# Kernel optimization log

Measured on AMD Instinct MI355X. Metric: run time of the kernel, lower is better.

Reference implementation:

```python
import jax, jax.numpy as jnp
import numpy as np

SEQ_LEN, HORIZON = 12, 12
B, N, DIN, DOUT, U = 16, 512, 2, 1, 64
NEG = -1e9


def _gat(x, W, a, b, mask):
    # x: (B, N, F_in); W: (F_in, G); a: (2, G); mask: (N, N) bool
    h = jnp.einsum('bnf,fg->bng', x, W)            # (B, N, G)
    src = jnp.einsum('bng,g->bn', h, a[0])         # (B, N)
    dst = jnp.einsum('bng,g->bn', h, a[1])         # (B, N)
    e = jax.nn.leaky_relu(src[:, :, None] + dst[:, None, :], 0.2)  # (B, N, N)
    e = jnp.where(mask[None], e, NEG)
    alpha = jax.nn.softmax(e, axis=-1)
    return jnp.einsum('bij,bjg->big', alpha, h) + b


def _cell(x, h_prev, W_ru, a_ru, b_ru, W_c, a_c, b_c, mask):
    # graph-attention GRU cell: x (B,N,Din), h_prev (B,N,U)
    xh = jnp.concatenate([x, h_prev], axis=-1)
    ru = jax.nn.sigmoid(_gat(xh, W_ru, a_ru, b_ru, mask))   # (B,N,2U)
    r, u = jnp.split(ru, 2, axis=-1)
    xc = jnp.concatenate([x, r * h_prev], axis=-1)
    c = jnp.tanh(_gat(xc, W_c, a_c, b_c, mask))
    return u * h_prev + (1.0 - u) * c


def setup_inputs() -> dict:
    key = jax.random.key(0)
    ks = jax.random.split(key, 16)
    s = 0.05
    inp = {
        'inputs': jax.random.normal(ks[0], (SEQ_LEN, B, N * DIN), jnp.float32),
        'adj': jax.random.uniform(ks[1], (N, N), jnp.float32),
        # encoder GAGRU cell (input_dim = DIN)
        'enc_W_ru': jax.random.normal(ks[2], (DIN + U, 2 * U), jnp.float32) * s,
        'enc_a_ru': jax.random.normal(ks[3], (2, 2 * U), jnp.float32) * s,
        'enc_b_ru': jnp.zeros((2 * U,), jnp.float32),
        'enc_W_c': jax.random.normal(ks[4], (DIN + U, U), jnp.float32) * s,
        'enc_a_c': jax.random.normal(ks[5], (2, U), jnp.float32) * s,
        'enc_b_c': jnp.zeros((U,), jnp.float32),
        # decoder GAGRU cell (input_dim = DOUT)
        'dec_W_ru': jax.random.normal(ks[6], (DOUT + U, 2 * U), jnp.float32) * s,
        'dec_a_ru': jax.random.normal(ks[7], (2, 2 * U), jnp.float32) * s,
        'dec_b_ru': jnp.zeros((2 * U,), jnp.float32),
        'dec_W_c': jax.random.normal(ks[8], (DOUT + U, U), jnp.float32) * s,
        'dec_a_c': jax.random.normal(ks[9], (2, U), jnp.float32) * s,
        'dec_b_c': jnp.zeros((U,), jnp.float32),
        # projection Linear(rnn_units -> output_dim)
        'proj_W': jax.random.normal(ks[10], (U, DOUT), jnp.float32) * s,
        'proj_b': jnp.zeros((DOUT,), jnp.float32),
    }
    return inp


def reference(inputs, adj, enc_W_ru, enc_a_ru, enc_b_ru, enc_W_c, enc_a_c, enc_b_c,
              dec_W_ru, dec_a_ru, dec_b_ru, dec_W_c, dec_a_c, dec_b_c, proj_W, proj_b):
    mask = (adj > 0.9) | jnp.eye(N, dtype=bool)
    x_seq = inputs.reshape(SEQ_LEN, B, N, DIN)

    # ---- encoder: scan GAGRU cell over seq_len ----
    def enc_step(h, x_t):
        h_new = _cell(x_t, h, enc_W_ru, enc_a_ru, enc_b_ru, enc_W_c, enc_a_c, enc_b_c, mask)
        return h_new, None

    h0 = jnp.zeros((B, N, U), inputs.dtype)
    h_enc, _ = jax.lax.scan(enc_step, h0, x_seq)

    def dec_step(carry, _):
        y_prev, h = carry
        h_new = _cell(y_prev, h, dec_W_ru, dec_a_ru, dec_b_ru, dec_W_c, dec_a_c, dec_b_c, mask)
        y = jnp.einsum('bnu,ud->bnd', h_new, proj_W) + proj_b  # (B, N, DOUT)
        return (y, h_new), y

    go = jnp.zeros((B, N, DOUT), inputs.dtype)
    _, outputs = jax.lax.scan(dec_step, (go, h_enc), None, length=HORIZON)
    return outputs  # (horizon, B, N, DOUT)
```

## Files before the change

kernel.cpp:

```cpp
#include <hip/hip_runtime.h>
#include <math.h>


#define NB 16
#define NN 512
#define NU 64
#define CAP 128
#define WPB 8

#define AS1 __attribute__((address_space(1)))
#define AS3 __attribute__((address_space(3)))

__device__ __forceinline__ void ld_lds16(float* lds_uniform, const float* g_perlane) {
#if __has_builtin(__builtin_amdgcn_global_load_lds)
  __builtin_amdgcn_global_load_lds((const AS1 unsigned int*)g_perlane,
                                   (AS3 unsigned int*)lds_uniform, 16, 0, 0);
#else
  int lane = threadIdx.x & 63;
  *(float4*)(lds_uniform + lane * 4) = *(const float4*)(g_perlane);
#endif
}

__device__ __forceinline__ void stage_weights(float* sW, const float* W, int TB,
                                              int w, int lane) {
  for (int c = w; c * 1024 < TB; c += WPB) {
    int off = c * 1024 + lane * 16;
    if (off < TB)
      ld_lds16((float*)((char*)sW + c * 1024), (const float*)((const char*)W + off));
  }
}

__device__ __forceinline__ float rlane(float v, int l) {
  return __int_as_float(__builtin_amdgcn_readlane(__float_as_int(v), l));
}
__device__ __forceinline__ int rlane_i(int v, int l) {
  return __builtin_amdgcn_readlane(v, l);
}
__device__ __forceinline__ float wave_max(float v) {
  #pragma unroll
  for (int s = 1; s < 64; s <<= 1) v = fmaxf(v, __shfl_xor(v, s));
  return v;
}
__device__ __forceinline__ float wave_sum(float v) {
  #pragma unroll
  for (int s = 1; s < 64; s <<= 1) v += __shfl_xor(v, s);
  return v;
}
__device__ __forceinline__ void wave_sum2(float& x, float& y) {
  #pragma unroll
  for (int s = 1; s < 64; s <<= 1) { x += __shfl_xor(x, s); y += __shfl_xor(y, s); }
}
__device__ __forceinline__ float fast_rcp(float x) {
#if __has_builtin(__builtin_amdgcn_rcpf)
  return __builtin_amdgcn_rcpf(x);
#else
  return 1.0f / x;
#endif
}
__device__ __forceinline__ float sigmoid_f(float x) {
  return fast_rcp(1.0f + __expf(-x));
}
__device__ __forceinline__ float tanh_f(float x) {
  return 1.0f - 2.0f * fast_rcp(__expf(2.0f * x) + 1.0f);
}

__device__ __forceinline__ void decode_block(int bx, int w, int& b, int& i) {
  int x = bx & 7, k = bx >> 3;
  b = (x << 1) | (k >> 6);
  i = ((k & 63) << 3) | w;
}

__global__ __launch_bounds__(64) void k_adj(const float* __restrict__ adj,
                                            int* __restrict__ cnt,
                                            int* __restrict__ idx) {
  int i = blockIdx.x;
  int l = threadIdx.x;
  int base = 0;
  #pragma unroll
  for (int c = 0; c < 8; ++c) {
    int j = c * 64 + l;
    bool pred = (adj[i * NN + j] > 0.9f) || (j == i);
    unsigned long long m = __ballot(pred);
    int pos = base + __popcll(m & ((1ull << l) - 1ull));
    if (pred && pos < CAP) idx[i * CAP + pos] = j;
    base += __popcll(m);
  }
  int total = base > CAP ? CAP : base;
  for (int p = total + l; p < CAP; p += 64) idx[i * CAP + p] = i;
  if (l == 0) cnt[i] = total;
}

template <int DIN>
__global__ __launch_bounds__(512, 6) void k_phaseB(
    const int* __restrict__ cnt, const int* __restrict__ idx,
    const float* __restrict__ h_ru, const float* __restrict__ src_ru,
    const float* __restrict__ dst_ru, const float* __restrict__ b_ru,
    const float* __restrict__ h, const float* __restrict__ x_ptr,
    const float* __restrict__ W_c, const float* __restrict__ a_c,
    float* __restrict__ h_c, float* __restrict__ src_c,
    float* __restrict__ dst_c, float* __restrict__ u_buf) {
  constexpr int TB = (DIN + NU) * NU * 4;
  __shared__ float sW[(DIN + NU) * NU];
  __shared__ float sh[WPB * NU];
  const int tid = threadIdx.x;
  const int w = tid >> 6, lane = tid & 63;

  stage_weights(sW, W_c, TB, w, lane);

  int b, i;
  decode_block(blockIdx.x, w, b, i);
  const int base_bi = (b << 9) + i;
  const float* __restrict__ hrb = h_ru + ((size_t)b << 16);
  const float* __restrict__ drb = dst_ru + (b << 9);

  const int c_ = cnt[i];
  const float si = src_ru[base_bi];
  const int j0 = idx[(i << 7) + lane];
  const int j1 = idx[(i << 7) + 64 + lane];
  float e0 = -1e30f, e1 = -1e30f;
  if (lane < c_)      { float t = si + drb[j0]; e0 = t >= 0.f ? t : 0.2f * t; }
  if (lane + 64 < c_) { float t = si + drb[j1]; e1 = t >= 0.f ? t : 0.2f * t; }
  float m = wave_max(fmaxf(e0, e1));
  float p0 = (lane < c_) ? __expf(e0 - m) : 0.f;
  float p1 = (lane + 64 < c_) ? __expf(e1 - m) : 0.f;
  float inv = fast_rcp(wave_sum(p0 + p1));
  p0 *= inv; p1 *= inv;

  const int g0 = lane << 1;
  float A0 = 0.f, A1 = 0.f, B0 = 0.f, B1 = 0.f;
  const int cc = (c_ + 15) & ~15;
  for (int base = 0; base < cc; base += 16) {
    float2 hv[16];
    #pragma unroll
    for (int q = 0; q < 16; ++q) {
      int jj = base + q;
      int sl = jj & 63;
      int j = (jj < 64) ? rlane_i(j0, sl) : rlane_i(j1, sl);
      hv[q] = *(const float2*)(hrb + (j << 7) + g0);
    }
    #pragma unroll
    for (int q = 0; q < 16; ++q) {
      int jj = base + q;
      int sl = jj & 63;
      float pv = (jj < 64) ? rlane(p0, sl) : rlane(p1, sl);
      if (q & 1) { B0 = fmaf(pv, hv[q].x, B0); B1 = fmaf(pv, hv[q].y, B1); }
      else       { A0 = fmaf(pv, hv[q].x, A0); A1 = fmaf(pv, hv[q].y, A1); }
    }
  }
  A0 += B0; A1 += B1;

  const float2 br = *(const float2*)(b_ru + g0);
  const float ru0 = sigmoid_f(A0 + br.x);
  const float ru1 = sigmoid_f(A1 + br.y);

  if (lane < 32) {
    float2 hh = *(const float2*)(h + ((size_t)base_bi << 6) + g0);
    *(float2*)&sh[(w << 6) + g0] = make_float2(ru0 * hh.x, ru1 * hh.y);
  } else {
    *(float2*)(u_buf + ((size_t)base_bi << 6) + (g0 - 64)) = make_float2(ru0, ru1);
  }

  __syncthreads();

  float acc;
  if (DIN == 2) {
    float2 xv = *(const float2*)(x_ptr + ((size_t)base_bi << 1));
    acc = xv.x * sW[lane];
    acc = fmaf(xv.y, sW[NU + lane], acc);
  } else {
    acc = x_ptr[base_bi] * sW[lane];
  }
  const float* __restrict__ sWh = sW + DIN * NU;
  const float* shw = sh + (w << 6);
  #pragma unroll
  for (int f2 = 0; f2 < 32; ++f2) {
    float2 rv = *(const float2*)(shw + 2 * f2);
    acc = fmaf(rv.x, sWh[(2 * f2) * NU + lane], acc);
    acc = fmaf(rv.y, sWh[(2 * f2 + 1) * NU + lane], acc);
  }
  h_c[((size_t)base_bi << 6) + lane] = acc;
  float s0 = acc * a_c[lane];
  float s1 = acc * a_c[NU + lane];
  wave_sum2(s0, s1);
  if (lane == 0) { src_c[base_bi] = s0; dst_c[base_bi] = s1; }
}

template <int UPD, int DIN_NEXT, int XMODE, int OUT>
__global__ __launch_bounds__(512, 8) void k_phaseA(
    const int* __restrict__ cnt, const int* __restrict__ idx,
    const float* __restrict__ h_c, const float* __restrict__ src_c,
    const float* __restrict__ dst_c, const float* __restrict__ b_c,
    const float* __restrict__ u_buf, float* __restrict__ h,
    const float* __restrict__ proj_W, const float* __restrict__ proj_b,
    float* __restrict__ out_slice, float* __restrict__ y_buf,
    const float* __restrict__ x_ptr,
    const float* __restrict__ W_ru, const float* __restrict__ a_ru,
    float* __restrict__ h_ru, float* __restrict__ src_ru,
    float* __restrict__ dst_ru) {
  constexpr int SWN = (DIN_NEXT > 0) ? (DIN_NEXT + NU) * 128 : 1;
  constexpr int TB = (DIN_NEXT > 0) ? SWN * 4 : 0;
  __shared__ float sW[SWN];
  __shared__ float sh[WPB * NU];
  const int tid = threadIdx.x;
  const int w = tid >> 6, lane = tid & 63;

  if (DIN_NEXT > 0) stage_weights(sW, W_ru, TB, w, lane);

  int b, i;
  decode_block(blockIdx.x, w, b, i);
  const int base_bi = (b << 9) + i;

  float hn = 0.f;
  if (UPD) {
    const float* __restrict__ hcb = h_c + ((size_t)b << 15);
    const float* __restrict__ dcb = dst_c + (b << 9);
    const int c_ = cnt[i];
    const float si = src_c[base_bi];
    const int j0 = idx[(i << 7) + lane];
    const int j1 = idx[(i << 7) + 64 + lane];
    float e0 = -1e30f, e1 = -1e30f;
    if (lane < c_)      { float t = si + dcb[j0]; e0 = t >= 0.f ? t : 0.2f * t; }
    if (lane + 64 < c_) { float t = si + dcb[j1]; e1 = t >= 0.f ? t : 0.2f * t; }
    float m = wave_max(fmaxf(e0, e1));
    float p0 = (lane < c_) ? __expf(e0 - m) : 0.f;
    float p1 = (lane + 64 < c_) ? __expf(e1 - m) : 0.f;
    float inv = fast_rcp(wave_sum(p0 + p1));
    p0 *= inv; p1 *= inv;

    float A = 0.f, Bacc = 0.f;
    const int cc = (c_ + 15) & ~15;
    for (int base = 0; base < cc; base += 16) {
      float hv[16];
      #pragma unroll
      for (int q = 0; q < 16; ++q) {
        int jj = base + q;
        int sl = jj & 63;
        int j = (jj < 64) ? rlane_i(j0, sl) : rlane_i(j1, sl);
        hv[q] = hcb[(j << 6) + lane];
      }
      #pragma unroll
      for (int q = 0; q < 16; ++q) {
        int jj = base + q;
        int sl = jj & 63;
        float pv = (jj < 64) ? rlane(p0, sl) : rlane(p1, sl);
        if (q & 1) Bacc = fmaf(pv, hv[q], Bacc);
        else       A = fmaf(pv, hv[q], A);
      }
    }
    A += Bacc;
    const float cc_ = tanh_f(A + b_c[lane]);
    const float u = u_buf[((size_t)base_bi << 6) + lane];
    const float ho = h[((size_t)base_bi << 6) + lane];
    hn = fmaf(u, ho - cc_, cc_);
  }
  h[((size_t)base_bi << 6) + lane] = hn;
  sh[(w << 6) + lane] = hn;

  float y = 0.f;
  if (OUT) {
    float t = wave_sum(hn * proj_W[lane]);
    y = t + proj_b[0];
    if (lane == 0) { out_slice[base_bi] = y; y_buf[base_bi] = y; }
  }

  if (DIN_NEXT > 0) {
    __syncthreads();
    const int g0 = lane << 1;
    float a0, a1;
    if (XMODE == 0) {
      if (DIN_NEXT == 2) {
        float2 xv = *(const float2*)(x_ptr + ((size_t)base_bi << 1));
        a0 = xv.x * sW[g0];
        a1 = xv.x * sW[g0 + 1];
        a0 = fmaf(xv.y, sW[128 + g0], a0);
        a1 = fmaf(xv.y, sW[128 + g0 + 1], a1);
      } else {
        float xv = x_ptr[base_bi];
        a0 = xv * sW[g0]; a1 = xv * sW[g0 + 1];
      }
    } else if (XMODE == 2) {
      a0 = y * sW[g0]; a1 = y * sW[g0 + 1];
    } else {
      a0 = 0.f; a1 = 0.f;
    }
    const float* __restrict__ sWh = sW + DIN_NEXT * 128;
    const float* shw = sh + (w << 6);
    #pragma unroll
    for (int f2 = 0; f2 < 32; ++f2) {
      float2 hp = *(const float2*)(shw + 2 * f2);
      float2 w0 = *(const float2*)(sWh + (2 * f2) * 128 + g0);
      float2 w1 = *(const float2*)(sWh + (2 * f2 + 1) * 128 + g0);
      a0 = fmaf(hp.x, w0.x, a0); a1 = fmaf(hp.x, w0.y, a1);
      a0 = fmaf(hp.y, w1.x, a0); a1 = fmaf(hp.y, w1.y, a1);
    }
    *(float2*)(h_ru + ((size_t)base_bi << 7) + g0) = make_float2(a0, a1);
    const float2 ar0 = *(const float2*)(a_ru + g0);
    const float2 ar1 = *(const float2*)(a_ru + 128 + g0);
    float s0 = a0 * ar0.x + a1 * ar0.y;
    float s1 = a0 * ar1.x + a1 * ar1.y;
    wave_sum2(s0, s1);
    if (lane == 0) { src_ru[base_bi] = s0; dst_ru[base_bi] = s1; }
  }
}

extern "C" void kernel_launch(void* const* d_in, const int* in_sizes, int n_in,
                              void* d_out, int out_size, void* d_ws, size_t ws_size,
                              hipStream_t stream) {
  (void)in_sizes; (void)n_in; (void)out_size; (void)ws_size;
  const float* inputs   = (const float*)d_in[0];
  const float* adj      = (const float*)d_in[1];
  const float* enc_W_ru = (const float*)d_in[2];
  const float* enc_a_ru = (const float*)d_in[3];
  const float* enc_b_ru = (const float*)d_in[4];
  const float* enc_W_c  = (const float*)d_in[5];
  const float* enc_a_c  = (const float*)d_in[6];
  const float* enc_b_c  = (const float*)d_in[7];
  const float* dec_W_ru = (const float*)d_in[8];
  const float* dec_a_ru = (const float*)d_in[9];
  const float* dec_b_ru = (const float*)d_in[10];
  const float* dec_W_c  = (const float*)d_in[11];
  const float* dec_a_c  = (const float*)d_in[12];
  const float* dec_b_c  = (const float*)d_in[13];
  const float* proj_W   = (const float*)d_in[14];
  const float* proj_b   = (const float*)d_in[15];
  float* out = (float*)d_out;

  char* ws = (char*)d_ws;
  int*   cnt    = (int*)ws;
  int*   idx    = (int*)(ws + 2048);
  float* h      = (float*)(ws + 264192);
  float* h_ru   = (float*)(ws + 2361344);
  float* src_ru = (float*)(ws + 6555648);
  float* dst_ru = (float*)(ws + 6588416);
  float* h_c    = (float*)(ws + 6621184);
  float* src_c  = (float*)(ws + 8718336);
  float* dst_c  = (float*)(ws + 8751104);
  float* u_buf  = (float*)(ws + 8783872);
  float* y_buf  = (float*)(ws + 10881024);

  hipMemsetAsync(y_buf, 0, NB * NN * sizeof(float), stream);
  k_adj<<<NN, 64, 0, stream>>>(adj, cnt, idx);

  const int GRID = (NB * NN) / WPB;

  k_phaseA<0, 2, 0, 0><<<GRID, 512, 0, stream>>>(cnt, idx, h_c, src_c, dst_c,
      enc_b_c, u_buf, h, proj_W, proj_b, nullptr, y_buf,
      inputs, enc_W_ru, enc_a_ru, h_ru, src_ru, dst_ru);

  for (int t = 0; t < 12; ++t) {
    k_phaseB<2><<<GRID, 512, 0, stream>>>(cnt, idx, h_ru, src_ru, dst_ru, enc_b_ru,
        h, inputs + (size_t)t * NB * NN * 2, enc_W_c, enc_a_c,
        h_c, src_c, dst_c, u_buf);
    if (t < 11)
      k_phaseA<1, 2, 0, 0><<<GRID, 512, 0, stream>>>(cnt, idx, h_c, src_c, dst_c,
          enc_b_c, u_buf, h, proj_W, proj_b, nullptr, y_buf,
          inputs + (size_t)(t + 1) * NB * NN * 2, enc_W_ru, enc_a_ru,
          h_ru, src_ru, dst_ru);
    else
      k_phaseA<1, 1, 1, 0><<<GRID, 512, 0, stream>>>(cnt, idx, h_c, src_c, dst_c,
          enc_b_c, u_buf, h, proj_W, proj_b, nullptr, y_buf,
          nullptr, dec_W_ru, dec_a_ru, h_ru, src_ru, dst_ru);
  }

  for (int k = 0; k < 12; ++k) {
    k_phaseB<1><<<GRID, 512, 0, stream>>>(cnt, idx, h_ru, src_ru, dst_ru, dec_b_ru,
        h, y_buf, dec_W_c, dec_a_c, h_c, src_c, dst_c, u_buf);
    if (k < 11)
      k_phaseA<1, 1, 2, 1><<<GRID, 512, 0, stream>>>(cnt, idx, h_c, src_c, dst_c,
          dec_b_c, u_buf, h, proj_W, proj_b, out + (size_t)k * NB * NN, y_buf,
          nullptr, dec_W_ru, dec_a_ru, h_ru, src_ru, dst_ru);
    else
      k_phaseA<1, 0, 1, 1><<<GRID, 512, 0, stream>>>(cnt, idx, h_c, src_c, dst_c,
          dec_b_c, u_buf, h, proj_W, proj_b, out + (size_t)k * NB * NN, y_buf,
          nullptr, dec_W_ru, dec_a_ru, h_ru, src_ru, dst_ru);
  }
}
```

Measured before the change: 802.2 us.

## Stage whole per-batch h_c slab in LDS for candidate-gate aggregation

Phase A now runs as 256 blocks, each handling 32 nodes of one batch. Each block first copies that batch's full 512x64 h_c matrix and its dst scores into LDS (about 128KB), so the neighbour gather reads LDS instead of scattered global memory. The same LDS buffer is then reused to stage the next step's W_ru before the r/u projection, and a separate k_init kernel handles the zero initial state. The aim is to cut repeated global gather traffic. The cost is far fewer blocks, lower occupancy, and an upfront full-slab load per block that is repeated across the 16 blocks sharing a batch.

```diff
diff --git a/kernel.cpp b/kernel.cpp
--- a/kernel.cpp
+++ b/kernel.cpp
@@ -21,12 +21,12 @@
 #endif
 }
 
-__device__ __forceinline__ void stage_weights(float* sW, const float* W, int TB,
-                                              int w, int lane) {
+__device__ __forceinline__ void stage_lds(float* dst, const float* src, int TB,
+                                          int w, int lane) {
   for (int c = w; c * 1024 < TB; c += WPB) {
     int off = c * 1024 + lane * 16;
     if (off < TB)
-      ld_lds16((float*)((char*)sW + c * 1024), (const float*)((const char*)W + off));
+      ld_lds16((float*)((char*)dst + c * 1024), (const float*)((const char*)src + off));
   }
 }
 
@@ -105,7 +105,7 @@
   const int tid = threadIdx.x;
   const int w = tid >> 6, lane = tid & 63;
 
-  stage_weights(sW, W_c, TB, w, lane);
+  stage_lds(sW, W_c, TB, w, lane);
 
   int b, i;
   decode_block(blockIdx.x, w, b, i);
@@ -185,8 +185,42 @@
   if (lane == 0) { src_c[base_bi] = s0; dst_c[base_bi] = s1; }
 }
 
-template <int UPD, int DIN_NEXT, int XMODE, int OUT>
-__global__ __launch_bounds__(512, 8) void k_phaseA(
+__global__ __launch_bounds__(512, 6) void k_init(
+    float* __restrict__ h, const float* __restrict__ x_ptr,
+    const float* __restrict__ W_ru, const float* __restrict__ a_ru,
+    float* __restrict__ h_ru, float* __restrict__ src_ru,
+    float* __restrict__ dst_ru) {
+  __shared__ float sW[66 * 128];
+  __shared__ float sh[WPB * NU];
+  const int tid = threadIdx.x;
+  const int w = tid >> 6, lane = tid & 63;
+  stage_lds(sW, W_ru, 66 * 128 * 4, w, lane);
+
+  int b, i;
+  decode_block(blockIdx.x, w, b, i);
+  const int base_bi = (b << 9) + i;
+
+  h[((size_t)base_bi << 6) + lane] = 0.f;
+  sh[(w << 6) + lane] = 0.f;
+  __syncthreads();
+
+  const int g0 = lane << 1;
+  float2 xv = *(const float2*)(x_ptr + ((size_t)base_bi << 1));
+  float a0 = xv.x * sW[g0];
+  float a1 = xv.x * sW[g0 + 1];
+  a0 = fmaf(xv.y, sW[128 + g0], a0);
+  a1 = fmaf(xv.y, sW[128 + g0 + 1], a1);
+  *(float2*)(h_ru + ((size_t)base_bi << 7) + g0) = make_float2(a0, a1);
+  const float2 ar0 = *(const float2*)(a_ru + g0);
+  const float2 ar1 = *(const float2*)(a_ru + 128 + g0);
+  float s0 = a0 * ar0.x + a1 * ar0.y;
+  float s1 = a0 * ar1.x + a1 * ar1.y;
+  wave_sum2(s0, s1);
+  if (lane == 0) { src_ru[base_bi] = s0; dst_ru[base_bi] = s1; }
+}
+
+template <int DIN_NEXT, int XMODE, int OUT>
+__global__ __launch_bounds__(512, 2) void k_phaseA2(
     const int* __restrict__ cnt, const int* __restrict__ idx,
     const float* __restrict__ h_c, const float* __restrict__ src_c,
     const float* __restrict__ dst_c, const float* __restrict__ b_c,
@@ -197,30 +231,35 @@
     const float* __restrict__ W_ru, const float* __restrict__ a_ru,
     float* __restrict__ h_ru, float* __restrict__ src_ru,
     float* __restrict__ dst_ru) {
-  constexpr int SWN = (DIN_NEXT > 0) ? (DIN_NEXT + NU) * 128 : 1;
-  constexpr int TB = (DIN_NEXT > 0) ? SWN * 4 : 0;
-  __shared__ float sW[SWN];
-  __shared__ float sh[WPB * NU];
+  __shared__ float lds_main[NN * NU];
+  __shared__ float sh[32 * NU];
+  __shared__ float sdst[NN];
+  __shared__ float sy[32];
   const int tid = threadIdx.x;
   const int w = tid >> 6, lane = tid & 63;
-
-  if (DIN_NEXT > 0) stage_weights(sW, W_ru, TB, w, lane);
-
-  int b, i;
-  decode_block(blockIdx.x, w, b, i);
-  const int base_bi = (b << 9) + i;
-
-  float hn = 0.f;
-  if (UPD) {
-    const float* __restrict__ hcb = h_c + ((size_t)b << 15);
-    const float* __restrict__ dcb = dst_c + (b << 9);
+  const int b = ((blockIdx.x & 7) << 1) | ((blockIdx.x >> 3) >> 4);
+  const int group = (blockIdx.x >> 3) & 15;
+
+  stage_lds(lds_main, h_c + ((size_t)b << 15), NN * NU * 4, w, lane);
+  if (w == 0) {
+    const char* s2 = (const char*)(dst_c + (b << 9));
+    ld_lds16(sdst, (const float*)(s2 + lane * 16));
+    ld_lds16(sdst + 256, (const float*)(s2 + 1024 + lane * 16));
+  }
+  __syncthreads();
+
+  for (int n = 0; n < 4; ++n) {
+    const int i = (group << 5) + (w << 2) + n;
+    const int bi = (b << 9) + i;
+    const float u_v = u_buf[((size_t)bi << 6) + lane];
+    const float ho  = h[((size_t)bi << 6) + lane];
     const int c_ = cnt[i];
-    const float si = src_c[base_bi];
+    const float si = src_c[bi];
     const int j0 = idx[(i << 7) + lane];
     const int j1 = idx[(i << 7) + 64 + lane];
     float e0 = -1e30f, e1 = -1e30f;
-    if (lane < c_)      { float t = si + dcb[j0]; e0 = t >= 0.f ? t : 0.2f * t; }
-    if (lane + 64 < c_) { float t = si + dcb[j1]; e1 = t >= 0.f ? t : 0.2f * t; }
+    if (lane < c_)      { float t = si + sdst[j0]; e0 = t >= 0.f ? t : 0.2f * t; }
+    if (lane + 64 < c_) { float t = si + sdst[j1]; e1 = t >= 0.f ? t : 0.2f * t; }
     float m = wave_max(fmaxf(e0, e1));
     float p0 = (lane < c_) ? __expf(e0 - m) : 0.f;
     float p1 = (lane + 64 < c_) ? __expf(e1 - m) : 0.f;
@@ -236,7 +275,7 @@
         int jj = base + q;
         int sl = jj & 63;
         int j = (jj < 64) ? rlane_i(j0, sl) : rlane_i(j1, sl);
-        hv[q] = hcb[(j << 6) + lane];
+        hv[q] = lds_main[(j << 6) + lane];
       }
       #pragma unroll
       for (int q = 0; q < 16; ++q) {
@@ -249,57 +288,59 @@
     }
     A += Bacc;
     const float cc_ = tanh_f(A + b_c[lane]);
-    const float u = u_buf[((size_t)base_bi << 6) + lane];
-    const float ho = h[((size_t)base_bi << 6) + lane];
-    hn = fmaf(u, ho - cc_, cc_);
-  }
-  h[((size_t)base_bi << 6) + lane] = hn;
-  sh[(w << 6) + lane] = hn;
-
-  float y = 0.f;
-  if (OUT) {
-    float t = wave_sum(hn * proj_W[lane]);
-    y = t + proj_b[0];
-    if (lane == 0) { out_slice[base_bi] = y; y_buf[base_bi] = y; }
+    const float hn = fmaf(u_v, ho - cc_, cc_);
+    h[((size_t)bi << 6) + lane] = hn;
+    sh[((w << 2) + n) * NU + lane] = hn;
+
+    if (OUT) {
+      float t2 = wave_sum(hn * proj_W[lane]);
+      float yv = t2 + proj_b[0];
+      if (lane == 0) {
+        out_slice[bi] = yv; y_buf[bi] = yv; sy[(w << 2) + n] = yv;
+      }
+    }
   }
 
   if (DIN_NEXT > 0) {
     __syncthreads();
+    stage_lds(lds_main, W_ru, (DIN_NEXT + NU) * 128 * 4, w, lane);
+    __syncthreads();
+
     const int g0 = lane << 1;
-    float a0, a1;
-    if (XMODE == 0) {
-      if (DIN_NEXT == 2) {
-        float2 xv = *(const float2*)(x_ptr + ((size_t)base_bi << 1));
-        a0 = xv.x * sW[g0];
-        a1 = xv.x * sW[g0 + 1];
-        a0 = fmaf(xv.y, sW[128 + g0], a0);
-        a1 = fmaf(xv.y, sW[128 + g0 + 1], a1);
+    for (int n = 0; n < 4; ++n) {
+      const int i = (group << 5) + (w << 2) + n;
+      const int bi = (b << 9) + i;
+      float a0, a1;
+      if (XMODE == 0) {
+        float2 xv = *(const float2*)(x_ptr + ((size_t)bi << 1));
+        a0 = xv.x * lds_main[g0];
+        a1 = xv.x * lds_main[g0 + 1];
+        a0 = fmaf(xv.y, lds_main[128 + g0], a0);
+        a1 = fmaf(xv.y, lds_main[128 + g0 + 1], a1);
+      } else if (XMODE == 2) {
+        float yv = sy[(w << 2) + n];
+        a0 = yv * lds_main[g0]; a1 = yv * lds_main[g0 + 1];
       } else {
-        float xv = x_ptr[base_bi];
-        a0 = xv * sW[g0]; a1 = xv * sW[g0 + 1];
+        a0 = 0.f; a1 = 0.f;
       }
-    } else if (XMODE == 2) {
-      a0 = y * sW[g0]; a1 = y * sW[g0 + 1];
-    } else {
-      a0 = 0.f; a1 = 0.f;
+      const float* sWh = lds_main + DIN_NEXT * 128;
+      const float* shw = sh + ((w << 2) + n) * NU;
+      #pragma unroll
+      for (int f2 = 0; f2 < 32; ++f2) {
+        float2 hp = *(const float2*)(shw + 2 * f2);
+        float2 w0 = *(const float2*)(sWh + (2 * f2) * 128 + g0);
+        float2 w1 = *(const float2*)(sWh + (2 * f2 + 1) * 128 + g0);
+        a0 = fmaf(hp.x, w0.x, a0); a1 = fmaf(hp.x, w0.y, a1);
+        a0 = fmaf(hp.y, w1.x, a0); a1 = fmaf(hp.y, w1.y, a1);
+      }
+      *(float2*)(h_ru + ((size_t)bi << 7) + g0) = make_float2(a0, a1);
+      const float2 ar0 = *(const float2*)(a_ru + g0);
+      const float2 ar1 = *(const float2*)(a_ru + 128 + g0);
+      float s0 = a0 * ar0.x + a1 * ar0.y;
+      float s1 = a0 * ar1.x + a1 * ar1.y;
+      wave_sum2(s0, s1);
+      if (lane == 0) { src_ru[bi] = s0; dst_ru[bi] = s1; }
     }
-    const float* __restrict__ sWh = sW + DIN_NEXT * 128;
-    const float* shw = sh + (w << 6);
-    #pragma unroll
-    for (int f2 = 0; f2 < 32; ++f2) {
-      float2 hp = *(const float2*)(shw + 2 * f2);
-      float2 w0 = *(const float2*)(sWh + (2 * f2) * 128 + g0);
-      float2 w1 = *(const float2*)(sWh + (2 * f2 + 1) * 128 + g0);
-      a0 = fmaf(hp.x, w0.x, a0); a1 = fmaf(hp.x, w0.y, a1);
-      a0 = fmaf(hp.y, w1.x, a0); a1 = fmaf(hp.y, w1.y, a1);
-    }
-    *(float2*)(h_ru + ((size_t)base_bi << 7) + g0) = make_float2(a0, a1);
-    const float2 ar0 = *(const float2*)(a_ru + g0);
-    const float2 ar1 = *(const float2*)(a_ru + 128 + g0);
-    float s0 = a0 * ar0.x + a1 * ar0.y;
-    float s1 = a0 * ar1.x + a1 * ar1.y;
-    wave_sum2(s0, s1);
-    if (lane == 0) { src_ru[base_bi] = s0; dst_ru[base_bi] = s1; }
   }
 }
 
@@ -342,22 +383,22 @@
   k_adj<<<NN, 64, 0, stream>>>(adj, cnt, idx);
 
   const int GRID = (NB * NN) / WPB;
-
-  k_phaseA<0, 2, 0, 0><<<GRID, 512, 0, stream>>>(cnt, idx, h_c, src_c, dst_c,
-      enc_b_c, u_buf, h, proj_W, proj_b, nullptr, y_buf,
-      inputs, enc_W_ru, enc_a_ru, h_ru, src_ru, dst_ru);
+  const int GRID2 = 256;
+
+  k_init<<<GRID, 512, 0, stream>>>(h, inputs, enc_W_ru, enc_a_ru,
+                                   h_ru, src_ru, dst_ru);
 
   for (int t = 0; t < 12; ++t) {
     k_phaseB<2><<<GRID, 512, 0, stream>>>(cnt, idx, h_ru, src_ru, dst_ru, enc_b_ru,
         h, inputs + (size_t)t * NB * NN * 2, enc_W_c, enc_a_c,
         h_c, src_c, dst_c, u_buf);
     if (t < 11)
-      k_phaseA<1, 2, 0, 0><<<GRID, 512, 0, stream>>>(cnt, idx, h_c, src_c, dst_c,
+      k_phaseA2<2, 0, 0><<<GRID2, 512, 0, stream>>>(cnt, idx, h_c, src_c, dst_c,
           enc_b_c, u_buf, h, proj_W, proj_b, nullptr, y_buf,
           inputs + (size_t)(t + 1) * NB * NN * 2, enc_W_ru, enc_a_ru,
           h_ru, src_ru, dst_ru);
     else
-      k_phaseA<1, 1, 1, 0><<<GRID, 512, 0, stream>>>(cnt, idx, h_c, src_c, dst_c,
+      k_phaseA2<1, 1, 0><<<GRID2, 512, 0, stream>>>(cnt, idx, h_c, src_c, dst_c,
           enc_b_c, u_buf, h, proj_W, proj_b, nullptr, y_buf,
           nullptr, dec_W_ru, dec_a_ru, h_ru, src_ru, dst_ru);
   }
@@ -366,11 +407,11 @@
     k_phaseB<1><<<GRID, 512, 0, stream>>>(cnt, idx, h_ru, src_ru, dst_ru, dec_b_ru,
         h, y_buf, dec_W_c, dec_a_c, h_c, src_c, dst_c, u_buf);
     if (k < 11)
-      k_phaseA<1, 1, 2, 1><<<GRID, 512, 0, stream>>>(cnt, idx, h_c, src_c, dst_c,
+      k_phaseA2<1, 2, 1><<<GRID2, 512, 0, stream>>>(cnt, idx, h_c, src_c, dst_c,
           dec_b_c, u_buf, h, proj_W, proj_b, out + (size_t)k * NB * NN, y_buf,
           nullptr, dec_W_ru, dec_a_ru, h_ru, src_ru, dst_ru);
     else
-      k_phaseA<1, 0, 1, 1><<<GRID, 512, 0, stream>>>(cnt, idx, h_c, src_c, dst_c,
+      k_phaseA2<0, 1, 1><<<GRID2, 512, 0, stream>>>(cnt, idx, h_c, src_c, dst_c,
           dec_b_c, u_buf, h, proj_W, proj_b, out + (size_t)k * NB * NN, y_buf,
           nullptr, dec_W_ru, dec_a_ru, h_ru, src_ru, dst_ru);
   }
```

New measurement: 856.8 us. 6.8% more time.
